# Optimization experiments

Hardware: AMD Instinct MI355X
Metric: run time of the kernel (lower is better)

The kernel has to match this reference:

```python
import jax, jax.numpy as jnp
import numpy as np

ALPHA = 1.0  # Student-t degrees of freedom (DEC default)


def setup_inputs() -> dict:
    key = jax.random.key(0)
    k1, k2 = jax.random.split(key)
    N, K, D = 32768, 1000, 1024
    h = jax.random.normal(k1, (N, D), dtype=jnp.float32)
    centroids = jax.random.normal(k2, (K, D), dtype=jnp.float32)
    return {"h": h, "centroids": centroids}


def reference(h, centroids):
    # squared pairwise L2 distance via the GEMM expansion:
    # ||h_i - mu_j||^2 = ||h_i||^2 + ||mu_j||^2 - 2 h_i . mu_j
    h_sq = jnp.sum(h * h, axis=1, keepdims=True)            # [N, 1]
    c_sq = jnp.sum(centroids * centroids, axis=1)           # [K]
    cross = jnp.einsum('nd,kd->nk', h, centroids)           # [N, K]
    d2 = jnp.maximum(h_sq + c_sq[None, :] - 2.0 * cross, 0.0)
    # Student-t kernel soft assignment (DEC):
    # q_ij = (1 + d2/alpha)^(-(alpha+1)/2) / sum_j'
    power = -(ALPHA + 1.0) / 2.0
    q = (1.0 + d2 / ALPHA) ** power                          # [N, K]
    q = q / jnp.sum(q, axis=1, keepdims=True)
    return q
```

## Files before the change

kernel.cpp:

```cpp
#include <hip/hip_runtime.h>


typedef unsigned short u16;
typedef __attribute__((ext_vector_type(8))) short bf16x8;
typedef __attribute__((ext_vector_type(4))) float f32x4;

#define N_ROWS 32768
#define K_CENT 1000
#define KP     1024
#define DDIM   1024

__device__ __forceinline__ u16 f2bf(float x) {
  unsigned u = __float_as_uint(x);
  u += 0x7fffu + ((u >> 16) & 1u);
  return (u16)(u >> 16);
}

__device__ __forceinline__ void gload_lds16(const u16* g, u16* s) {
  __builtin_amdgcn_global_load_lds((__attribute__((address_space(1))) void*)g,
                                   (__attribute__((address_space(3))) void*)s,
                                   16, 0, 0);
}


__global__ __launch_bounds__(256) void prep_h(const float* __restrict__ h,
                                              u16* __restrict__ hb,
                                              float* __restrict__ hsq,
                                              float* __restrict__ rowsum) {
  const int row = blockIdx.x;
  const int t = threadIdx.x;
  const float4 v = reinterpret_cast<const float4*>(h + (size_t)row * DDIM)[t];
  ushort4 b;
  b.x = f2bf(v.x); b.y = f2bf(v.y); b.z = f2bf(v.z); b.w = f2bf(v.w);
  reinterpret_cast<ushort4*>(hb + (size_t)row * DDIM)[t] = b;
  float ss = v.x * v.x + v.y * v.y + v.z * v.z + v.w * v.w;
#pragma unroll
  for (int m = 1; m < 64; m <<= 1) ss += __shfl_xor(ss, m);
  __shared__ float sbuf[4];
  if ((t & 63) == 0) sbuf[t >> 6] = ss;
  __syncthreads();
  if (t == 0) {
    hsq[row] = sbuf[0] + sbuf[1] + sbuf[2] + sbuf[3];
    rowsum[row] = 0.0f;
  }
}

__global__ __launch_bounds__(256) void prep_c(const float* __restrict__ c,
                                              u16* __restrict__ cb,
                                              float* __restrict__ csq) {
  const int row = blockIdx.x;
  const int t = threadIdx.x;
  if (row < K_CENT) {
    const float4 v = reinterpret_cast<const float4*>(c + (size_t)row * DDIM)[t];
    ushort4 b;
    b.x = f2bf(v.x); b.y = f2bf(v.y); b.z = f2bf(v.z); b.w = f2bf(v.w);
    reinterpret_cast<ushort4*>(cb + (size_t)row * DDIM)[t] = b;
    float ss = v.x * v.x + v.y * v.y + v.z * v.z + v.w * v.w;
#pragma unroll
    for (int m = 1; m < 64; m <<= 1) ss += __shfl_xor(ss, m);
    __shared__ float sbuf[4];
    if ((t & 63) == 0) sbuf[t >> 6] = ss;
    __syncthreads();
    if (t == 0) csq[row] = sbuf[0] + sbuf[1] + sbuf[2] + sbuf[3];
  } else {
    ushort4 z; z.x = z.y = z.z = z.w = 0;
    reinterpret_cast<ushort4*>(cb + (size_t)row * DDIM)[t] = z;
    if (t == 0) csq[row] = 1e30f;
  }
}


__device__ __forceinline__ void stage_tile(const u16* __restrict__ gA,
                                           const u16* __restrict__ gB,
                                           u16* sA, u16* sB,
                                           int w, int l, int k0) {
#pragma unroll
  for (int i = 0; i < 2; ++i) {
    const int c = w + i * 4;
    const int roff = c * 16 + (l >> 2);
    const int koff = (l & 3) * 8;
    const size_t go = (size_t)roff * DDIM + k0 + koff;
    gload_lds16(gA + go, sA + c * 512);
    gload_lds16(gB + go, sB + c * 512);
  }
}

__global__ __launch_bounds__(256) void gemm_q(const u16* __restrict__ hb,
                                              const u16* __restrict__ cb,
                                              const float* __restrict__ hsq,
                                              const float* __restrict__ csq,
                                              float* __restrict__ out,
                                              float* __restrict__ rowsum) {
  __shared__ u16 As[2][128 * 32];
  __shared__ u16 Bs[2][128 * 32];

  const int bid = blockIdx.x;
  const int swz = ((bid & 7) << 8) | (bid >> 3);
  const int bcol = swz & 7;
  const int brow = swz >> 3;

  const int t = threadIdx.x;
  const int w = t >> 6;
  const int l = t & 63;
  const int wr = w >> 1;
  const int wc = w & 1;

  const u16* gA = hb + (size_t)brow * 128 * DDIM;
  const u16* gB = cb + (size_t)bcol * 128 * DDIM;

  f32x4 acc[4][4] = {};

  stage_tile(gA, gB, &As[0][0], &Bs[0][0], w, l, 0);

  const int NT = DDIM / 32;
  for (int kt = 0; kt < NT; ++kt) {
    const int cur = kt & 1;
    __syncthreads();
    if (kt + 1 < NT)
      stage_tile(gA, gB, &As[cur ^ 1][0], &Bs[cur ^ 1][0], w, l, (kt + 1) * 32);

    bf16x8 aF[4], bF[4];
#pragma unroll
    for (int m = 0; m < 4; ++m) {
      aF[m] = *(const bf16x8*)&As[cur][(wr * 64 + m * 16 + (l & 15)) * 32 + (l >> 4) * 8];
      bF[m] = *(const bf16x8*)&Bs[cur][(wc * 64 + m * 16 + (l & 15)) * 32 + (l >> 4) * 8];
    }
#pragma unroll
    for (int m = 0; m < 4; ++m)
#pragma unroll
      for (int n = 0; n < 4; ++n)
        acc[m][n] = __builtin_amdgcn_mfma_f32_16x16x32_bf16(aF[m], bF[n], acc[m][n], 0, 0, 0);
  }

  const int gi0 = brow * 128 + wr * 64;
  const int gj0 = bcol * 128 + wc * 64;
  const int lr = (l >> 4) << 2;
  const int lc = l & 15;

#pragma unroll
  for (int m = 0; m < 4; ++m) {
    float hs[4];
#pragma unroll
    for (int r = 0; r < 4; ++r) hs[r] = hsq[gi0 + m * 16 + lr + r];
    float rs[4] = {0.f, 0.f, 0.f, 0.f};
#pragma unroll
    for (int n = 0; n < 4; ++n) {
      const int gj = gj0 + n * 16 + lc;
      const float cs = csq[gj];
#pragma unroll
      for (int r = 0; r < 4; ++r) {
        float d2 = hs[r] + cs - 2.0f * acc[m][n][r];
        d2 = fmaxf(d2, 0.0f);
        const float qv = 1.0f / (1.0f + d2);
        rs[r] += qv;
        if (gj < K_CENT)
          out[(size_t)(gi0 + m * 16 + lr + r) * K_CENT + gj] = qv;
      }
    }
#pragma unroll
    for (int r = 0; r < 4; ++r) {
      float v = rs[r];
      v += __shfl_xor(v, 1);
      v += __shfl_xor(v, 2);
      v += __shfl_xor(v, 4);
      v += __shfl_xor(v, 8);
      if (lc == 0) atomicAdd(&rowsum[gi0 + m * 16 + lr + r], v);
    }
  }
}


__global__ __launch_bounds__(256) void norm_k(float* __restrict__ out,
                                              const float* __restrict__ rowsum) {
  const int row = blockIdx.x;
  const int t = threadIdx.x;
  if (t < 250) {
    const float inv = 1.0f / rowsum[row];
    float4* p = reinterpret_cast<float4*>(out) + (size_t)row * 250 + t;
    float4 v = *p;
    v.x *= inv; v.y *= inv; v.z *= inv; v.w *= inv;
    *p = v;
  }
}


extern "C" void kernel_launch(void* const* d_in, const int* in_sizes, int n_in,
                              void* d_out, int out_size, void* d_ws, size_t ws_size,
                              hipStream_t stream) {
  const float* h   = (const float*)d_in[0];
  const float* cen = (const float*)d_in[1];
  float* out = (float*)d_out;
  char* ws = (char*)d_ws;

  u16*   cb     = (u16*)(ws);
  u16*   hb     = (u16*)(ws + 2097152);
  float* hsq    = (float*)(ws + 2097152 + 67108864);
  float* csq    = (float*)(ws + 2097152 + 67108864 + 131072);
  float* rowsum = (float*)(ws + 2097152 + 67108864 + 131072 + 4096);

  prep_c<<<KP, 256, 0, stream>>>(cen, cb, csq);
  prep_h<<<N_ROWS, 256, 0, stream>>>(h, hb, hsq, rowsum);
  gemm_q<<<(N_ROWS / 128) * (KP / 128), 256, 0, stream>>>(hb, cb, hsq, csq, out, rowsum);
  norm_k<<<N_ROWS, 256, 0, stream>>>(out, rowsum);
}
```

Measured before the change: 192.1 us.

## Keep full-depth centroid slab resident in LDS and stream h from global

The GEMM kernel now loads a whole 64-centroid by 1024-depth bf16 slab into LDS once per block, using an XOR swizzle to avoid bank conflicts. Each of 8 waves handles 64 rows of h and reads its A fragments directly from global memory into registers, double-buffered across k-tiles, with MFMA priority raised. This removes the per-k-tile A/B LDS staging and barriers. In exchange it uses 128KB of LDS per block, which limits occupancy, and relies on cache hits for h rows that are reloaded once per centroid column block (16 times).

```diff
diff --git a/kernel.cpp b/kernel.cpp
--- a/kernel.cpp
+++ b/kernel.cpp
@@ -9,6 +9,7 @@
 #define K_CENT 1000
 #define KP     1024
 #define DDIM   1024
+#define NT     32
 
 __device__ __forceinline__ u16 f2bf(float x) {
   unsigned u = __float_as_uint(x);
@@ -70,82 +71,97 @@
 }
 
 
-__device__ __forceinline__ void stage_tile(const u16* __restrict__ gA,
-                                           const u16* __restrict__ gB,
-                                           u16* sA, u16* sB,
-                                           int w, int l, int k0) {
-#pragma unroll
-  for (int i = 0; i < 2; ++i) {
-    const int c = w + i * 4;
-    const int roff = c * 16 + (l >> 2);
-    const int koff = (l & 3) * 8;
-    const size_t go = (size_t)roff * DDIM + k0 + koff;
-    gload_lds16(gA + go, sA + c * 512);
-    gload_lds16(gB + go, sB + c * 512);
-  }
-}
-
-__global__ __launch_bounds__(256) void gemm_q(const u16* __restrict__ hb,
+__global__ __launch_bounds__(512) void gemm_b(const u16* __restrict__ hb,
                                               const u16* __restrict__ cb,
                                               const float* __restrict__ hsq,
                                               const float* __restrict__ csq,
                                               float* __restrict__ out,
                                               float* __restrict__ rowsum) {
-  __shared__ u16 As[2][128 * 32];
-  __shared__ u16 Bs[2][128 * 32];
+  __shared__ u16 Bs[64 * DDIM];
 
   const int bid = blockIdx.x;
-  const int swz = ((bid & 7) << 8) | (bid >> 3);
-  const int bcol = swz & 7;
-  const int brow = swz >> 3;
-
-  const int t = threadIdx.x;
-  const int w = t >> 6;
-  const int l = t & 63;
-  const int wr = w >> 1;
-  const int wc = w & 1;
-
-  const u16* gA = hb + (size_t)brow * 128 * DDIM;
-  const u16* gB = cb + (size_t)bcol * 128 * DDIM;
+  const int swz = ((bid & 7) << 7) | (bid >> 3);
+  const int bcol = swz & 15;
+  const int brow = swz >> 4;
+
+  const int tid = threadIdx.x;
+  const int w = tid >> 6;
+  const int l = tid & 63;
+
+  const u16* gB = cb + (size_t)bcol * 64 * DDIM;
+
+#pragma unroll
+  for (int i = 0; i < 16; ++i) {
+    const int p = w * 64 + i * 512 + l;
+    const int g = p ^ ((p >> 7) & 7);
+    gload_lds16(gB + (size_t)(g >> 7) * DDIM + (g & 127) * 8,
+                Bs + ((w * 64 + i * 512) << 3));
+  }
+
+  const int row0 = brow * 512 + w * 64;
+  const u16* gA = hb + (size_t)row0 * DDIM;
+
+  const int hi = l >> 4;
+  const u16* gAm[4];
+#pragma unroll
+  for (int m = 0; m < 4; ++m)
+    gAm[m] = gA + (size_t)(m * 16 + (l & 15)) * DDIM + hi * 8;
+
+  int cbase[4], cx[4];
+#pragma unroll
+  for (int n = 0; n < 4; ++n) {
+    const int col_loc = n * 16 + (l & 15);
+    cbase[n] = col_loc * 128;
+    cx[n] = col_loc & 7;
+  }
+
+  asm volatile("s_waitcnt vmcnt(0)" ::: "memory");
+  __syncthreads();
 
   f32x4 acc[4][4] = {};
-
-  stage_tile(gA, gB, &As[0][0], &Bs[0][0], w, l, 0);
-
-  const int NT = DDIM / 32;
-  for (int kt = 0; kt < NT; ++kt) {
-    const int cur = kt & 1;
-    __syncthreads();
-    if (kt + 1 < NT)
-      stage_tile(gA, gB, &As[cur ^ 1][0], &Bs[cur ^ 1][0], w, l, (kt + 1) * 32);
-
-    bf16x8 aF[4], bF[4];
-#pragma unroll
-    for (int m = 0; m < 4; ++m) {
-      aF[m] = *(const bf16x8*)&As[cur][(wr * 64 + m * 16 + (l & 15)) * 32 + (l >> 4) * 8];
-      bF[m] = *(const bf16x8*)&Bs[cur][(wc * 64 + m * 16 + (l & 15)) * 32 + (l >> 4) * 8];
-    }
-#pragma unroll
-    for (int m = 0; m < 4; ++m)
-#pragma unroll
-      for (int n = 0; n < 4; ++n)
-        acc[m][n] = __builtin_amdgcn_mfma_f32_16x16x32_bf16(aF[m], bF[n], acc[m][n], 0, 0, 0);
-  }
-
-  const int gi0 = brow * 128 + wr * 64;
-  const int gj0 = bcol * 128 + wc * 64;
-  const int lr = (l >> 4) << 2;
+  bf16x8 a0[4], a1[4];
+
+#define LOADA(SET, T)                                                          \
+  _Pragma("unroll") for (int m = 0; m < 4; ++m)                                \
+      SET[m] = *(const bf16x8*)(gAm[m] + (T) * 32);
+
+#define TILE(T, SET)                                                           \
+  {                                                                            \
+    const int t4 = (T) * 4;                                                    \
+    bf16x8 bF[4];                                                              \
+    _Pragma("unroll") for (int n = 0; n < 4; ++n)                              \
+        bF[n] = *(const bf16x8*)&Bs[(cbase[n] + ((t4 + hi) ^ cx[n])) << 3];    \
+    __builtin_amdgcn_s_setprio(1);                                             \
+    _Pragma("unroll") for (int m = 0; m < 4; ++m)                              \
+      _Pragma("unroll") for (int n = 0; n < 4; ++n)                            \
+        acc[m][n] = __builtin_amdgcn_mfma_f32_16x16x32_bf16(SET[m], bF[n],     \
+                                                            acc[m][n], 0, 0, 0); \
+    __builtin_amdgcn_s_setprio(0);                                             \
+  }
+
+  LOADA(a0, 0)
+#pragma unroll 1
+  for (int t = 0; t < NT; t += 2) {
+    LOADA(a1, t + 1)
+    TILE(t, a0)
+    if (t + 2 < NT) LOADA(a0, t + 2)
+    TILE(t + 1, a1)
+  }
+#undef LOADA
+#undef TILE
+
+  const int lr = hi << 2;
   const int lc = l & 15;
 
 #pragma unroll
   for (int m = 0; m < 4; ++m) {
     float hs[4];
 #pragma unroll
-    for (int r = 0; r < 4; ++r) hs[r] = hsq[gi0 + m * 16 + lr + r];
+    for (int r = 0; r < 4; ++r) hs[r] = hsq[row0 + m * 16 + lr + r];
     float rs[4] = {0.f, 0.f, 0.f, 0.f};
 #pragma unroll
     for (int n = 0; n < 4; ++n) {
-      const int gj = gj0 + n * 16 + lc;
+      const int gj = bcol * 64 + n * 16 + lc;
       const float cs = csq[gj];
 #pragma unroll
       for (int r = 0; r < 4; ++r) {
@@ -154,7 +170,7 @@
         const float qv = 1.0f / (1.0f + d2);
         rs[r] += qv;
         if (gj < K_CENT)
-          out[(size_t)(gi0 + m * 16 + lr + r) * K_CENT + gj] = qv;
+          out[(size_t)(row0 + m * 16 + lr + r) * K_CENT + gj] = qv;
       }
     }
 #pragma unroll
@@ -164,7 +180,7 @@
       v += __shfl_xor(v, 2);
       v += __shfl_xor(v, 4);
       v += __shfl_xor(v, 8);
-      if (lc == 0) atomicAdd(&rowsum[gi0 + m * 16 + lr + r], v);
+      if (lc == 0) atomicAdd(&rowsum[row0 + m * 16 + lr + r], v);
     }
   }
 }
@@ -200,6 +216,6 @@
 
   prep_c<<<KP, 256, 0, stream>>>(cen, cb, csq);
   prep_h<<<N_ROWS, 256, 0, stream>>>(h, hb, hsq, rowsum);
-  gemm_q<<<(N_ROWS / 128) * (KP / 128), 256, 0, stream>>>(hb, cb, hsq, csq, out, rowsum);
+  gemm_b<<<(N_ROWS / 512) * (KP / 64), 512, 0, stream>>>(hb, cb, hsq, csq, out, rowsum);
   norm_k<<<N_ROWS, 256, 0, stream>>>(out, rowsum);
 }
```

New measurement: 244.6 us. +27.3%, slower.
